# Performance work log

Measured on AMD Instinct MI355X. Metric: run time of the kernel, lower is better.

Reference implementation:

```python
import jax, jax.numpy as jnp
import numpy as np

B, N, K, C_IN, C_OUT = 4, 8192, 32, 64, 64
MID = (C_OUT + C_IN) // 2  # 64, since C_IN is even
GROUPS = 8
EPS = 1e-5
SLOPE = 0.1


def group_norm(x, gamma, beta, groups=GROUPS, eps=EPS):
    # x: [b, ..., C], normalize per-sample over all spatial dims and group channels
    b = x.shape[0]
    C = x.shape[-1]
    xr = x.reshape(b, -1, groups, C // groups)
    mean = xr.mean(axis=(1, 3), keepdims=True)
    var = xr.var(axis=(1, 3), keepdims=True)
    xn = ((xr - mean) / jnp.sqrt(var + eps)).reshape(x.shape)
    return xn * gamma + beta


def lrelu(x):
    return jnp.where(x >= 0, x, SLOPE * x)


def setup_inputs() -> dict:
    key = jax.random.key(0)
    ks = jax.random.split(key, 10)
    signal = jax.random.normal(ks[0], (B, N, C_IN), dtype=jnp.float32)
    edges = jax.random.randint(ks[1], (B * N * K,), 0, B * N, dtype=jnp.int64)
    edge_feats = jax.random.normal(ks[2], (B * N * K, 3), dtype=jnp.float32)
    W1 = jax.random.normal(ks[3], (MID, C_IN + 3), dtype=jnp.float32) * 0.1
    W2 = jax.random.normal(ks[4], (C_OUT, MID), dtype=jnp.float32) * 0.1
    W3 = jax.random.normal(ks[5], (C_OUT, C_OUT), dtype=jnp.float32) * 0.1
    return {
        "signal": signal, "edges": edges, "edge_feats": edge_feats,
        "W1": W1, "g1": jnp.ones((MID,), jnp.float32), "b1": jnp.zeros((MID,), jnp.float32),
        "W2": W2, "g2": jnp.ones((C_OUT,), jnp.float32), "b2": jnp.zeros((C_OUT,), jnp.float32),
        "W3": W3, "g3": jnp.ones((C_OUT,), jnp.float32), "b3": jnp.zeros((C_OUT,), jnp.float32),
    }


def reference(signal, edges, edge_feats, W1, g1, b1, W2, g2, b2, W3, g3, b3):
    b, n, c = signal.shape
    k = edges.shape[0] // (b * n)
    flat = signal.reshape(b * n, c)
    # gather neighbor features and take relative difference: [b*n, k, c]
    ef = flat[edges].reshape(b * n, k, c) - flat[:, None, :]
    # concat relative coordinates -> [b, n, k, c+3]
    x = jnp.concatenate([ef, edge_feats.reshape(b * n, k, 3)], axis=-1)
    x = x.reshape(b, n, k, c + 3)
    # 1x1 conv (fc1) + GN + lrelu
    x = jnp.einsum('bnkc,mc->bnkm', x, W1)
    x = lrelu(group_norm(x, g1, b1))
    # max-pool over neighbors -> [b, n, mid]
    x = jnp.max(x, axis=2)
    # fc2 + GN + lrelu
    x = jnp.einsum('bnm,om->bno', x, W2)
    x = lrelu(group_norm(x, g2, b2))
    # fc3 + GN + lrelu
    x = jnp.einsum('bno,po->bnp', x, W3)
    x = lrelu(group_norm(x, g3, b3))
    return x  # [b, n, nb_feat_out]
```

## Files before the change

### kernel.cpp

```cpp
#include <hip/hip_runtime.h>

#define NB    4
#define NPB   8192
#define NPTS  (NB*NPB)
#define KNB   32
#define CH    64
#define W1C   67
#define GRPS  8
#define EPSV  1e-5f
#define SLOPEV 0.1f

typedef float f32x4 __attribute__((ext_vector_type(4)));
typedef short bf16x8 __attribute__((ext_vector_type(8)));
typedef unsigned short u16;
typedef u16 u16x4 __attribute__((ext_vector_type(4)));
typedef u16 u16x8 __attribute__((ext_vector_type(8)));

#define WS_STATS1 0
#define WS_STATS2 64
#define WS_STATS3 128
#define WS_FLAG   192
#define WS_YB     256
#define WS_MX     (WS_YB + NPTS*CH/2)
#define WS_MN     (WS_MX + NPTS*CH)

#define LDP 72

__device__ __forceinline__ u16 f2bf(float f) {
    unsigned u = __float_as_uint(f);
    u += 0x7fff + ((u >> 16) & 1);
    return (u16)(u >> 16);
}
__device__ __forceinline__ float bf2f(u16 h) {
    return __uint_as_float(((unsigned)h) << 16);
}

template<int MODE>
__global__ __launch_bounds__(256) void k_mm(
    const void* __restrict__ X0,
    const float* __restrict__ X1,
    const float* __restrict__ Wg,
    const float* __restrict__ statsIn, float invcnt,
    const float* __restrict__ gm, const float* __restrict__ bt,
    void* __restrict__ Out,
    float* __restrict__ statsOut,
    const int* __restrict__ e_i32, int* __restrict__ flag)
{
    __shared__ u16 Al[128*LDP];
    __shared__ u16 Wl[64*LDP];
    __shared__ float affA[64], affB[64];
    __shared__ float lacc[16];
    __shared__ int sfnd[4];
    int tid = threadIdx.x;
    int pbase = blockIdx.x * 128;
    int b = pbase >> 13;

    if (MODE == 0 && blockIdx.x == 0) {
        if (tid < 192) statsOut[tid] = 0.f;
        int found = 0;
        #pragma unroll
        for (int i = 0; i < 16; ++i) {
            int idx = ((tid << 4) + i) * 2 + 1;
            found |= (e_i32[idx] != 0);
        }
        unsigned long long bl = __ballot(found);
        if ((tid & 63) == 0) sfnd[tid >> 6] = (bl != 0ull) ? 1 : 0;
    }
    if (MODE != 0) {
        if (tid < 64) {
            int g = tid >> 3;
            float sv = statsIn[b*16 + g*2 + 0];
            float qv = statsIn[b*16 + g*2 + 1];
            float mean = sv * invcnt;
            float var  = fmaf(-mean, mean, qv * invcnt);
            float rstd = rsqrtf(var + EPSV);
            float a = gm[tid] * rstd;
            affA[tid] = a;
            affB[tid] = fmaf(-mean, a, bt[tid]);
        }
    }
    if (tid < 16) lacc[tid] = 0.f;
    __syncthreads();
    if (MODE == 0 && blockIdx.x == 0 && tid == 0)
        *flag = sfnd[0] | sfnd[1] | sfnd[2] | sfnd[3];

    {
        const int wstride = (MODE == 0) ? W1C : 64;
        #pragma unroll
        for (int i = 0; i < 16; ++i) {
            int e = tid + 256*i;
            int o = e >> 6, m = e & 63;
            Wl[o*LDP + m] = f2bf(Wg[o*wstride + m]);
        }
    }
    #pragma unroll
    for (int it = 0; it < 8; ++it) {
        int fi = it*1024 + tid*4;
        int p = fi >> 6;
        int m = fi & 63;
        float xv[4];
        if (MODE == 1) {
            f32x4 vx = *(const f32x4*)&((const float*)X0)[(pbase+p)*64 + m];
            f32x4 vn = *(const f32x4*)&X1[(pbase+p)*64 + m];
            #pragma unroll
            for (int j = 0; j < 4; ++j) {
                float a = affA[m+j];
                float x = (a < 0.f) ? vn[j] : vx[j];
                float z = fmaf(a, x, affB[m+j]);
                xv[j] = (z >= 0.f) ? z : SLOPEV * z;
            }
        } else if (MODE == 2) {
            u16x4 vh = *(const u16x4*)&((const u16*)X0)[(pbase+p)*64 + m];
            #pragma unroll
            for (int j = 0; j < 4; ++j) {
                float z = fmaf(affA[m+j], bf2f(vh[j]), affB[m+j]);
                xv[j] = (z >= 0.f) ? z : SLOPEV * z;
            }
        } else {
            f32x4 vx = *(const f32x4*)&((const float*)X0)[(pbase+p)*64 + m];
            #pragma unroll
            for (int j = 0; j < 4; ++j) xv[j] = vx[j];
        }
        #pragma unroll
        for (int j = 0; j < 4; ++j)
            Al[p*LDP + m + j] = f2bf(xv[j]);
    }
    __syncthreads();

    int l = tid & 63, w = tid >> 6;
    int lr = l & 15;
    int lk = l >> 4;
    bf16x8 af[2][2], bw[4][2];
    #pragma unroll
    for (int pt = 0; pt < 2; ++pt)
        #pragma unroll
        for (int kh = 0; kh < 2; ++kh)
            af[pt][kh] = *(const bf16x8*)&Al[(w*32 + pt*16 + lr)*LDP + kh*32 + lk*8];
    #pragma unroll
    for (int ot = 0; ot < 4; ++ot)
        #pragma unroll
        for (int kh = 0; kh < 2; ++kh)
            bw[ot][kh] = *(const bf16x8*)&Wl[(ot*16 + lr)*LDP + kh*32 + lk*8];

    f32x4 acc[2][4];
    #pragma unroll
    for (int pt = 0; pt < 2; ++pt)
        #pragma unroll
        for (int ot = 0; ot < 4; ++ot) {
            f32x4 c = {0.f, 0.f, 0.f, 0.f};
            c = __builtin_amdgcn_mfma_f32_16x16x32_bf16(af[pt][0], bw[ot][0], c, 0, 0, 0);
            c = __builtin_amdgcn_mfma_f32_16x16x32_bf16(af[pt][1], bw[ot][1], c, 0, 0, 0);
            acc[pt][ot] = c;
        }

    #pragma unroll
    for (int pt = 0; pt < 2; ++pt)
        #pragma unroll
        for (int ot = 0; ot < 4; ++ot)
            #pragma unroll
            for (int r = 0; r < 4; ++r) {
                int p = pbase + w*32 + pt*16 + lk*4 + r;
                int o = ot*16 + lr;
                if (MODE == 2) ((float*)Out)[p*64 + o] = acc[pt][ot][r];
                else           ((u16*)Out)[p*64 + o]  = f2bf(acc[pt][ot][r]);
            }

    if (MODE != 0) {
        #pragma unroll
        for (int ot = 0; ot < 4; ++ot) {
            float s = 0.f, ss = 0.f;
            #pragma unroll
            for (int pt = 0; pt < 2; ++pt)
                #pragma unroll
                for (int r = 0; r < 4; ++r) {
                    float v = acc[pt][ot][r];
                    s += v;
                    ss = fmaf(v, v, ss);
                }
            s += __shfl_xor(s, 16, 64);  ss += __shfl_xor(ss, 16, 64);
            s += __shfl_xor(s, 32, 64);  ss += __shfl_xor(ss, 32, 64);
            s += __shfl_xor(s, 1, 64);   ss += __shfl_xor(ss, 1, 64);
            s += __shfl_xor(s, 2, 64);   ss += __shfl_xor(ss, 2, 64);
            s += __shfl_xor(s, 4, 64);   ss += __shfl_xor(ss, 4, 64);
            if ((l & 7) == 0 && l < 16) {
                int g = ot*2 + (l >> 3);
                atomicAdd(&lacc[g*2 + 0], s);
                atomicAdd(&lacc[g*2 + 1], ss);
            }
        }
        __syncthreads();
        if (tid < 16)
            atomicAdd(&statsOut[b*16 + tid], lacc[tid]);
    }
}

template<bool IS32>
__device__ __forceinline__ void edge_loop8(const u16* __restrict__ Yb,
    const void* __restrict__ edg, const float* __restrict__ ef,
    int p, int il, const float (&yp)[8],
    const float (&w0)[8], const float (&w1)[8], const float (&w2)[8],
    float (&mx)[8], float (&mn)[8], float& s, float& ss)
{
    const int*       e32 = (const int*)edg;
    const long long* e64 = (const long long*)edg;
    #pragma unroll 4
    for (int k = 0; k < KNB; ++k) {
        int ei = p*KNB + k;
        int e  = IS32 ? __builtin_nontemporal_load(e32 + ei)
                      : (int)__builtin_nontemporal_load(e64 + ei);
        float c0 = __builtin_nontemporal_load(ef + ei*3 + 0);
        float c1 = __builtin_nontemporal_load(ef + ei*3 + 1);
        float c2 = __builtin_nontemporal_load(ef + ei*3 + 2);
        u16x8 q = *(const u16x8*)&Yb[e*64 + il*8];
        #pragma unroll
        for (int j = 0; j < 8; ++j) {
            float t = fmaf(c2, w2[j], fmaf(c1, w1[j], fmaf(c0, w0[j], bf2f(q[j]) - yp[j])));
            mx[j] = fmaxf(mx[j], t);
            mn[j] = fminf(mn[j], t);
            s += t;
            ss = fmaf(t, t, ss);
        }
    }
}

#define PPB_E 32
__global__ __launch_bounds__(256) void k_edge(const u16* __restrict__ Yb,
    const void* __restrict__ edg, const float* __restrict__ ef,
    const float* __restrict__ W1, const int* __restrict__ flag,
    float* __restrict__ Mx, float* __restrict__ Mn, float* __restrict__ stats1)
{
    __shared__ float lacc[16];
    int tid = threadIdx.x, lane = tid & 63, wv = tid >> 6;
    int il = lane & 7;
    int g8 = lane >> 3;
    if (tid < 16) lacc[tid] = 0.f;

    int p = blockIdx.x * PPB_E + wv * 8 + g8;

    float w0[8], w1[8], w2[8], yp[8], mx[8], mn[8];
    #pragma unroll
    for (int j = 0; j < 8; ++j) {
        int ch = il*8 + j;
        w0[j] = W1[ch*W1C + 64];
        w1[j] = W1[ch*W1C + 65];
        w2[j] = W1[ch*W1C + 66];
    }
    u16x8 yh = *(const u16x8*)&Yb[p*64 + il*8];
    #pragma unroll
    for (int j = 0; j < 8; ++j) {
        yp[j] = bf2f(yh[j]);
        mx[j] = -3.4e38f;
        mn[j] =  3.4e38f;
    }
    float s = 0.f, ss = 0.f;
    bool is32 = (*flag != 0);
    __syncthreads();

    if (is32) edge_loop8<true >(Yb, edg, ef, p, il, yp, w0, w1, w2, mx, mn, s, ss);
    else      edge_loop8<false>(Yb, edg, ef, p, il, yp, w0, w1, w2, mx, mn, s, ss);

    f32x4 mxa = {mx[0], mx[1], mx[2], mx[3]};
    f32x4 mxb = {mx[4], mx[5], mx[6], mx[7]};
    f32x4 mna = {mn[0], mn[1], mn[2], mn[3]};
    f32x4 mnb = {mn[4], mn[5], mn[6], mn[7]};
    __builtin_nontemporal_store(mxa, (f32x4*)(Mx + p*64 + il*8));
    __builtin_nontemporal_store(mxb, (f32x4*)(Mx + p*64 + il*8 + 4));
    __builtin_nontemporal_store(mna, (f32x4*)(Mn + p*64 + il*8));
    __builtin_nontemporal_store(mnb, (f32x4*)(Mn + p*64 + il*8 + 4));

    s += __shfl_xor(s,  8, 64);  ss += __shfl_xor(ss,  8, 64);
    s += __shfl_xor(s, 16, 64);  ss += __shfl_xor(ss, 16, 64);
    s += __shfl_xor(s, 32, 64);  ss += __shfl_xor(ss, 32, 64);
    if (lane < 8) {
        atomicAdd(&lacc[lane*2 + 0], s);
        atomicAdd(&lacc[lane*2 + 1], ss);
    }
    __syncthreads();
    if (tid < 16) {
        int b = (blockIdx.x * PPB_E) / NPB;
        atomicAdd(&stats1[b*16 + tid], lacc[tid]);
    }
}

__global__ __launch_bounds__(256) void k_out(const float* __restrict__ Vpre,
    const float* __restrict__ stats, float invcnt,
    const float* __restrict__ gm, const float* __restrict__ bt,
    float* __restrict__ out)
{
    int idx = blockIdx.x * blockDim.x + threadIdx.x;
    int p  = idx >> 4;
    int m0 = (idx & 15) << 2;
    int b  = p >> 13;
    int g  = m0 >> 3;
    float sv = stats[b*16 + g*2 + 0];
    float qv = stats[b*16 + g*2 + 1];
    float mean = sv * invcnt;
    float var  = fmaf(-mean, mean, qv * invcnt);
    float rstd = rsqrtf(var + EPSV);
    float4 v = reinterpret_cast<const float4*>(Vpre)[idx];
    float in[4] = {v.x, v.y, v.z, v.w};
    float r[4];
    #pragma unroll
    for (int j = 0; j < 4; ++j) {
        float aa = gm[m0+j] * rstd;
        float z  = fmaf(aa, in[j] - mean, bt[m0+j]);
        r[j] = (z >= 0.f) ? z : SLOPEV * z;
    }
    float4 o4 = {r[0], r[1], r[2], r[3]};
    reinterpret_cast<float4*>(out)[idx] = o4;
}

extern "C" void kernel_launch(void* const* d_in, const int* in_sizes, int n_in,
                              void* d_out, int out_size, void* d_ws, size_t ws_size,
                              hipStream_t stream)
{
    const float* sig = (const float*)d_in[0];
    const void*  edg = d_in[1];
    const float* ef  = (const float*)d_in[2];
    const float* W1  = (const float*)d_in[3];
    const float* g1  = (const float*)d_in[4];
    const float* b1  = (const float*)d_in[5];
    const float* W2  = (const float*)d_in[6];
    const float* g2  = (const float*)d_in[7];
    const float* b2  = (const float*)d_in[8];
    const float* W3  = (const float*)d_in[9];
    const float* g3  = (const float*)d_in[10];
    const float* b3  = (const float*)d_in[11];
    float* out = (float*)d_out;
    float* ws  = (float*)d_ws;
    u16*   yb  = (u16*)(ws + WS_YB);

    k_mm<0><<<NPTS/128, 256, 0, stream>>>(sig, nullptr, W1, nullptr, 0.f,
                                          nullptr, nullptr, yb, ws,
                                          (const int*)edg, (int*)(ws + WS_FLAG));
    k_edge<<<NPTS/PPB_E, 256, 0, stream>>>(yb, edg, ef, W1,
                                           (const int*)(ws + WS_FLAG),
                                           ws + WS_MX, ws + WS_MN, ws + WS_STATS1);
    k_mm<1><<<NPTS/128, 256, 0, stream>>>(ws + WS_MX, ws + WS_MN, W2,
                                          ws + WS_STATS1, 1.f/(float)(NPB*KNB*8),
                                          g1, b1, yb, ws + WS_STATS2,
                                          nullptr, nullptr);
    k_mm<2><<<NPTS/128, 256, 0, stream>>>(yb, nullptr, W3,
                                          ws + WS_STATS2, 1.f/(float)(NPB*8),
                                          g2, b2, ws + WS_MX, ws + WS_STATS3,
                                          nullptr, nullptr);
    k_out<<<(NPTS*CH/4)/256, 256, 0, stream>>>(ws + WS_MX, ws + WS_STATS3,
                                         1.f/(float)(NPB*8), g3, b3, out);
}
```

Before: 63.94 us.

## Store intermediates as bf16 and stage edge indices/features in shared memory

The per-point max/min buffers and the fc3 pre-activation output are stored as bf16 instead of fp32, which halves intermediate traffic between kernels. The edge kernel now cooperatively loads each block's edge indices and edge features into LDS with coalesced loads, and stores the pre-scaled byte offset. The inner loop then reads one float4 from LDS per neighbor instead of four scattered global loads. This adds bf16 rounding to the max/min and pre-GN3 values, which may slightly reduce accuracy.

```diff
diff --git a/kernel.cpp b/kernel.cpp
--- a/kernel.cpp
+++ b/kernel.cpp
@@ -22,7 +22,7 @@
 #define WS_FLAG   192
 #define WS_YB     256
 #define WS_MX     (WS_YB + NPTS*CH/2)
-#define WS_MN     (WS_MX + NPTS*CH)
+#define WS_MN     (WS_MX + NPTS*CH/2)
 
 #define LDP 72
 
@@ -38,7 +38,7 @@
 template<int MODE>
 __global__ __launch_bounds__(256) void k_mm(
     const void* __restrict__ X0,
-    const float* __restrict__ X1,
+    const void* __restrict__ X1,
     const float* __restrict__ Wg,
     const float* __restrict__ statsIn, float invcnt,
     const float* __restrict__ gm, const float* __restrict__ bt,
@@ -100,12 +100,12 @@
         int m = fi & 63;
         float xv[4];
         if (MODE == 1) {
-            f32x4 vx = *(const f32x4*)&((const float*)X0)[(pbase+p)*64 + m];
-            f32x4 vn = *(const f32x4*)&X1[(pbase+p)*64 + m];
+            u16x4 vx = *(const u16x4*)&((const u16*)X0)[(pbase+p)*64 + m];
+            u16x4 vn = *(const u16x4*)&((const u16*)X1)[(pbase+p)*64 + m];
             #pragma unroll
             for (int j = 0; j < 4; ++j) {
                 float a = affA[m+j];
-                float x = (a < 0.f) ? vn[j] : vx[j];
+                float x = (a < 0.f) ? bf2f(vn[j]) : bf2f(vx[j]);
                 float z = fmaf(a, x, affB[m+j]);
                 xv[j] = (z >= 0.f) ? z : SLOPEV * z;
             }
@@ -161,8 +161,7 @@
             for (int r = 0; r < 4; ++r) {
                 int p = pbase + w*32 + pt*16 + lk*4 + r;
                 int o = ot*16 + lr;
-                if (MODE == 2) ((float*)Out)[p*64 + o] = acc[pt][ot][r];
-                else           ((u16*)Out)[p*64 + o]  = f2bf(acc[pt][ot][r]);
+                ((u16*)Out)[p*64 + o] = f2bf(acc[pt][ot][r]);
             }
 
     if (MODE != 0) {
@@ -194,24 +193,69 @@
     }
 }
 
-template<bool IS32>
-__device__ __forceinline__ void edge_loop8(const u16* __restrict__ Yb,
+#define PPB_E 32
+#define SEDS  (KNB*4 + 4)
+__global__ __launch_bounds__(256) void k_edge(const u16* __restrict__ Yb,
     const void* __restrict__ edg, const float* __restrict__ ef,
-    int p, int il, const float (&yp)[8],
-    const float (&w0)[8], const float (&w1)[8], const float (&w2)[8],
-    float (&mx)[8], float (&mn)[8], float& s, float& ss)
+    const float* __restrict__ W1, const int* __restrict__ flag,
+    u16* __restrict__ Mx, u16* __restrict__ Mn, float* __restrict__ stats1)
 {
-    const int*       e32 = (const int*)edg;
-    const long long* e64 = (const long long*)edg;
-    #pragma unroll 4
+    __shared__ float sed[PPB_E*SEDS];
+    __shared__ float lacc[16];
+    int tid = threadIdx.x;
+    if (tid < 16) lacc[tid] = 0.f;
+
+    {
+        bool is32 = (*flag != 0);
+        const int*       e32 = (const int*)edg;
+        const long long* e64 = (const long long*)edg;
+        int ebase = blockIdx.x * (PPB_E*KNB);
+        #pragma unroll
+        for (int i = 0; i < 4; ++i) {
+            int idx = tid + i*256;
+            int gi  = ebase + idx;
+            int e   = is32 ? __builtin_nontemporal_load(e32 + gi)
+                           : (int)__builtin_nontemporal_load(e64 + gi);
+            int pt = idx >> 5, k = idx & 31;
+            float* d = &sed[pt*SEDS + k*4];
+            d[0] = __builtin_nontemporal_load(ef + gi*3 + 0);
+            d[1] = __builtin_nontemporal_load(ef + gi*3 + 1);
+            d[2] = __builtin_nontemporal_load(ef + gi*3 + 2);
+            d[3] = __int_as_float(e << 7);
+        }
+    }
+
+    int lane = tid & 63, wv = tid >> 6;
+    int il = lane & 7;
+    int g8 = lane >> 3;
+    int lpt = wv*8 + g8;
+    int p = blockIdx.x * PPB_E + lpt;
+
+    float w0[8], w1[8], w2[8], yp[8], mx[8], mn[8];
+    #pragma unroll
+    for (int j = 0; j < 8; ++j) {
+        int ch = il*8 + j;
+        w0[j] = W1[ch*W1C + 64];
+        w1[j] = W1[ch*W1C + 65];
+        w2[j] = W1[ch*W1C + 66];
+    }
+    u16x8 yh = *(const u16x8*)&Yb[p*64 + il*8];
+    #pragma unroll
+    for (int j = 0; j < 8; ++j) {
+        yp[j] = bf2f(yh[j]);
+        mx[j] = -3.4e38f;
+        mn[j] =  3.4e38f;
+    }
+    float s = 0.f, ss = 0.f;
+    __syncthreads();
+
+    const char* Ybase = (const char*)Yb + il*16;
+    const float* sp = &sed[lpt*SEDS];
+    #pragma unroll 8
     for (int k = 0; k < KNB; ++k) {
-        int ei = p*KNB + k;
-        int e  = IS32 ? __builtin_nontemporal_load(e32 + ei)
-                      : (int)__builtin_nontemporal_load(e64 + ei);
-        float c0 = __builtin_nontemporal_load(ef + ei*3 + 0);
-        float c1 = __builtin_nontemporal_load(ef + ei*3 + 1);
-        float c2 = __builtin_nontemporal_load(ef + ei*3 + 2);
-        u16x8 q = *(const u16x8*)&Yb[e*64 + il*8];
+        f32x4 m4 = *(const f32x4*)(sp + k*4);
+        u16x8 q = *(const u16x8*)(Ybase + __float_as_int(m4[3]));
+        float c0 = m4[0], c1 = m4[1], c2 = m4[2];
         #pragma unroll
         for (int j = 0; j < 8; ++j) {
             float t = fmaf(c2, w2[j], fmaf(c1, w1[j], fmaf(c0, w0[j], bf2f(q[j]) - yp[j])));
@@ -221,52 +265,12 @@
             ss = fmaf(t, t, ss);
         }
     }
-}
-
-#define PPB_E 32
-__global__ __launch_bounds__(256) void k_edge(const u16* __restrict__ Yb,
-    const void* __restrict__ edg, const float* __restrict__ ef,
-    const float* __restrict__ W1, const int* __restrict__ flag,
-    float* __restrict__ Mx, float* __restrict__ Mn, float* __restrict__ stats1)
-{
-    __shared__ float lacc[16];
-    int tid = threadIdx.x, lane = tid & 63, wv = tid >> 6;
-    int il = lane & 7;
-    int g8 = lane >> 3;
-    if (tid < 16) lacc[tid] = 0.f;
-
-    int p = blockIdx.x * PPB_E + wv * 8 + g8;
-
-    float w0[8], w1[8], w2[8], yp[8], mx[8], mn[8];
-    #pragma unroll
-    for (int j = 0; j < 8; ++j) {
-        int ch = il*8 + j;
-        w0[j] = W1[ch*W1C + 64];
-        w1[j] = W1[ch*W1C + 65];
-        w2[j] = W1[ch*W1C + 66];
-    }
-    u16x8 yh = *(const u16x8*)&Yb[p*64 + il*8];
-    #pragma unroll
-    for (int j = 0; j < 8; ++j) {
-        yp[j] = bf2f(yh[j]);
-        mx[j] = -3.4e38f;
-        mn[j] =  3.4e38f;
-    }
-    float s = 0.f, ss = 0.f;
-    bool is32 = (*flag != 0);
-    __syncthreads();
-
-    if (is32) edge_loop8<true >(Yb, edg, ef, p, il, yp, w0, w1, w2, mx, mn, s, ss);
-    else      edge_loop8<false>(Yb, edg, ef, p, il, yp, w0, w1, w2, mx, mn, s, ss);
-
-    f32x4 mxa = {mx[0], mx[1], mx[2], mx[3]};
-    f32x4 mxb = {mx[4], mx[5], mx[6], mx[7]};
-    f32x4 mna = {mn[0], mn[1], mn[2], mn[3]};
-    f32x4 mnb = {mn[4], mn[5], mn[6], mn[7]};
-    __builtin_nontemporal_store(mxa, (f32x4*)(Mx + p*64 + il*8));
-    __builtin_nontemporal_store(mxb, (f32x4*)(Mx + p*64 + il*8 + 4));
-    __builtin_nontemporal_store(mna, (f32x4*)(Mn + p*64 + il*8));
-    __builtin_nontemporal_store(mnb, (f32x4*)(Mn + p*64 + il*8 + 4));
+
+    u16x8 hx, hn;
+    #pragma unroll
+    for (int j = 0; j < 8; ++j) { hx[j] = f2bf(mx[j]); hn[j] = f2bf(mn[j]); }
+    __builtin_nontemporal_store(hx, (u16x8*)(Mx + p*64 + il*8));
+    __builtin_nontemporal_store(hn, (u16x8*)(Mn + p*64 + il*8));
 
     s += __shfl_xor(s,  8, 64);  ss += __shfl_xor(ss,  8, 64);
     s += __shfl_xor(s, 16, 64);  ss += __shfl_xor(ss, 16, 64);
@@ -282,7 +286,7 @@
     }
 }
 
-__global__ __launch_bounds__(256) void k_out(const float* __restrict__ Vpre,
+__global__ __launch_bounds__(256) void k_out(const u16* __restrict__ Vpre,
     const float* __restrict__ stats, float invcnt,
     const float* __restrict__ gm, const float* __restrict__ bt,
     float* __restrict__ out)
@@ -297,17 +301,16 @@
     float mean = sv * invcnt;
     float var  = fmaf(-mean, mean, qv * invcnt);
     float rstd = rsqrtf(var + EPSV);
-    float4 v = reinterpret_cast<const float4*>(Vpre)[idx];
-    float in[4] = {v.x, v.y, v.z, v.w};
+    u16x4 v = *(const u16x4*)&Vpre[idx*4];
     float r[4];
     #pragma unroll
     for (int j = 0; j < 4; ++j) {
         float aa = gm[m0+j] * rstd;
-        float z  = fmaf(aa, in[j] - mean, bt[m0+j]);
+        float z  = fmaf(aa, bf2f(v[j]) - mean, bt[m0+j]);
         r[j] = (z >= 0.f) ? z : SLOPEV * z;
     }
-    float4 o4 = {r[0], r[1], r[2], r[3]};
-    reinterpret_cast<float4*>(out)[idx] = o4;
+    f32x4 o4 = {r[0], r[1], r[2], r[3]};
+    *(f32x4*)&out[idx*4] = o4;
 }
 
 extern "C" void kernel_launch(void* const* d_in, const int* in_sizes, int n_in,
@@ -329,21 +332,23 @@
     float* out = (float*)d_out;
     float* ws  = (float*)d_ws;
     u16*   yb  = (u16*)(ws + WS_YB);
+    u16*   mxb = (u16*)(ws + WS_MX);
+    u16*   mnb = (u16*)(ws + WS_MN);
 
     k_mm<0><<<NPTS/128, 256, 0, stream>>>(sig, nullptr, W1, nullptr, 0.f,
                                           nullptr, nullptr, yb, ws,
                                           (const int*)edg, (int*)(ws + WS_FLAG));
     k_edge<<<NPTS/PPB_E, 256, 0, stream>>>(yb, edg, ef, W1,
                                            (const int*)(ws + WS_FLAG),
-                                           ws + WS_MX, ws + WS_MN, ws + WS_STATS1);
-    k_mm<1><<<NPTS/128, 256, 0, stream>>>(ws + WS_MX, ws + WS_MN, W2,
+                                           mxb, mnb, ws + WS_STATS1);
+    k_mm<1><<<NPTS/128, 256, 0, stream>>>(mxb, mnb, W2,
                                           ws + WS_STATS1, 1.f/(float)(NPB*KNB*8),
                                           g1, b1, yb, ws + WS_STATS2,
                                           nullptr, nullptr);
     k_mm<2><<<NPTS/128, 256, 0, stream>>>(yb, nullptr, W3,
                                           ws + WS_STATS2, 1.f/(float)(NPB*8),
-                                          g2, b2, ws + WS_MX, ws + WS_STATS3,
+                                          g2, b2, mxb, ws + WS_STATS3,
                                           nullptr, nullptr);
-    k_out<<<(NPTS*CH/4)/256, 256, 0, stream>>>(ws + WS_MX, ws + WS_STATS3,
+    k_out<<<(NPTS*CH/4)/256, 256, 0, stream>>>(mxb, ws + WS_STATS3,
                                          1.f/(float)(NPB*8), g3, b3, out);
 }
```

After: 56.86 us. 1.12x faster.
